# Kernel optimization log

Hardware: AMD Instinct MI355X
Metric: run time of the kernel (lower is better)

Reference implementation:

```python
import jax, jax.numpy as jnp
import numpy as np

EPS = 1e-5

def conv2d(x, w, b=None, stride=1, pad=0):
    # x: NCHW, w: OIHW
    y = jax.lax.conv_general_dilated(x, w, (stride, stride), [(pad, pad), (pad, pad)],
                                     dimension_numbers=('NCHW', 'OIHW', 'NCHW'))
    if b is not None:
        y = y + b[None, :, None, None]
    return y

def bn_eval(x, g, b, m, v):
    inv = jax.lax.rsqrt(v + EPS)
    return (x - m[None, :, None, None]) * (g * inv)[None, :, None, None] + b[None, :, None, None]

def setup_inputs() -> dict:
    key = jax.random.key(0)
    ks = jax.random.split(key, 20)
    B, Cin, Cout, H, W = 2, 64, 64, 96, 96
    Cqk = Cout // 4
    d = {}
    d['x'] = jax.random.normal(ks[0], (B, Cin, H, W), jnp.float32)
    # pre_conv: 3x3 conv (no bias) + BN + ReLU
    d['w_pre'] = jax.random.normal(ks[1], (Cout, Cin, 3, 3), jnp.float32) * 0.05
    d['bn1_g'] = jax.random.normal(ks[2], (Cout,), jnp.float32) * 0.1 + 1.0
    d['bn1_b'] = jax.random.normal(ks[3], (Cout,), jnp.float32) * 0.1
    d['bn1_m'] = jax.random.normal(ks[4], (Cout,), jnp.float32) * 0.1
    d['bn1_v'] = jax.random.uniform(ks[5], (Cout,), jnp.float32) + 0.5
    # 1x1 q/k/v convs (with bias, as nn.Conv2d default)
    d['wq'] = jax.random.normal(ks[6], (Cqk, Cout, 1, 1), jnp.float32) * 0.05
    d['bq'] = jax.random.normal(ks[7], (Cqk,), jnp.float32) * 0.01
    d['wk'] = jax.random.normal(ks[8], (Cqk, Cout, 1, 1), jnp.float32) * 0.05
    d['bk'] = jax.random.normal(ks[9], (Cqk,), jnp.float32) * 0.01
    d['wv'] = jax.random.normal(ks[10], (Cout, Cout, 1, 1), jnp.float32) * 0.05
    d['bv'] = jax.random.normal(ks[11], (Cout,), jnp.float32) * 0.01
    # final_conv: 3x3 conv (no bias) + BN + ReLU
    d['w_fin'] = jax.random.normal(ks[12], (Cout, Cout, 3, 3), jnp.float32) * 0.05
    d['bn2_g'] = jax.random.normal(ks[13], (Cout,), jnp.float32) * 0.1 + 1.0
    d['bn2_b'] = jax.random.normal(ks[14], (Cout,), jnp.float32) * 0.1
    d['bn2_m'] = jax.random.normal(ks[15], (Cout,), jnp.float32) * 0.1
    d['bn2_v'] = jax.random.uniform(ks[16], (Cout,), jnp.float32) + 0.5
    d['gamma'] = jnp.array([0.5], jnp.float32)  # nonzero so attention path contributes
    return d

def reference(x, w_pre, bn1_g, bn1_b, bn1_m, bn1_v, wq, bq, wk, bk, wv, bv,
              w_fin, bn2_g, bn2_b, bn2_m, bn2_v, gamma):
    # pre_conv: Conv3x3 + BN(eval) + ReLU
    x = jax.nn.relu(bn_eval(conv2d(x, w_pre, None, 1, 1), bn1_g, bn1_b, bn1_m, bn1_v))
    B, C, H, W = x.shape
    N = H * W
    q = conv2d(x, wq, bq).reshape(B, -1, N)   # (B, C/4, N)
    k = conv2d(x, wk, bk).reshape(B, -1, N)   # (B, C/4, N)
    v = conv2d(x, wv, bv).reshape(B, C, N)    # (B, C, N)
    energy = jnp.einsum('bci,bcj->bij', q, k)         # (B, N, N)
    attn = jax.nn.softmax(energy, axis=-1)
    # out[b,c,i] = sum_j v[b,c,j] * attn[b,i,j]  (bmm(V, attn^T) in torch)
    out = jnp.einsum('bcj,bij->bci', v, attn).reshape(B, C, H, W)
    out_feat = gamma[0] * out + x
    out_feat = jax.nn.relu(bn_eval(conv2d(out_feat, w_fin, None, 1, 1), bn2_g, bn2_b, bn2_m, bn2_v))
    return out_feat
```

## Files before the change

### kernel.cpp

```cpp
#include <hip/hip_runtime.h>
#include <hip/hip_bf16.h>


using short8 = __attribute__((ext_vector_type(8))) short;
using f32x4  = __attribute__((ext_vector_type(4))) float;
using f32x16 = __attribute__((ext_vector_type(16))) float;
using u32x4  = __attribute__((ext_vector_type(4))) unsigned;
typedef unsigned u32;
typedef unsigned short ushort;

#define NPIX 9216
#define PW 98
#define PLANE 9604
#define PLANEB 9608
#define SEG 240
#define LOG2E 1.44269504088896340736f

__device__ __forceinline__ ushort f2bf(float f) {
  u32 x = __builtin_bit_cast(u32, f);
  return (ushort)((x + 0x7fffu + ((x >> 16) & 1u)) >> 16);
}
__device__ __forceinline__ float bf2f(ushort h) {
  return __builtin_bit_cast(float, (u32)h << 16);
}

__global__ __launch_bounds__(256) void wprep(
    const float* __restrict__ w_pre, const float* __restrict__ w_fin,
    ushort* __restrict__ fpre, ushort* __restrict__ ffin)
{
  const int i = blockIdx.x * 256 + threadIdx.x;
  const float* w = blockIdx.y ? w_fin : w_pre;
  ushort* dst    = blockIdx.y ? ffin : fpre;
  const int kk = i & 7, l = (i >> 3) & 63, cot = (i >> 9) & 1;
  const int chunk = (i >> 10) & 3, tap = i >> 12;
  const int co = cot * 32 + (l & 31);
  const int ci = chunk * 16 + 8 * (l >> 5) + kk;
  const float wv = w[co * 576 + ci * 9 + tap];
  const ushort h = f2bf(wv);
  const ushort lo = f2bf(wv - bf2f(h));
  const int base = tap * 8192 + chunk * 2048 + cot * 1024 + l * 8 + kk;
  dst[base] = h;
  dst[base + 512] = lo;
}

__global__ __launch_bounds__(256) void pad_split(
    const float* __restrict__ in, ushort* __restrict__ xh, ushort* __restrict__ xl)
{
  const int plane = blockIdx.x;
  const float* src = in + (size_t)plane * 9216;
  const size_t dbase = (size_t)plane * PLANEB;
  for (int idx = threadIdx.x; idx < 9216; idx += 256) {
    const int y = idx / 96, x = idx - y * 96;
    const float v = src[idx];
    const ushort h = f2bf(v);
    const size_t d = dbase + (y + 1) * PW + x + 1;
    xh[d] = h;
    xl[d] = f2bf(v - bf2f(h));
  }
}

template <bool PADOUT>
__global__ __launch_bounds__(128) void conv3x3_mfma(
    const ushort* __restrict__ xh, const ushort* __restrict__ xl,
    const ushort* __restrict__ wfrag,
    const float* __restrict__ gg, const float* __restrict__ bb_,
    const float* __restrict__ mm, const float* __restrict__ vv,
    float* __restrict__ outp)
{
  __shared__ ushort stage[2][SEG][18];
  __shared__ float scb[64], shb[64];
  const int n0  = blockIdx.x * 32;
  const int b   = blockIdx.y;
  const int tid = threadIdx.x;
  const int wm  = tid >> 6;
  const int lane = tid & 63;
  const int li = lane & 31, hi = lane >> 5;

  if (tid < 64) {
    const float sc = gg[tid] * rsqrtf(vv[tid] + 1e-5f);
    scb[tid] = sc;
    shb[tid] = bb_[tid] - mm[tid] * sc;
  }

  f32x16 acc = {};
  const int sbase = n0 - 8;

  for (int chunk = 0; chunk < 4; ++chunk) {
    __syncthreads();
#pragma unroll
    for (int it = 0; it < 8; ++it) {
      const int item = tid + it * 128;
      if (item < 960) {
        const int pl   = item >= 480;
        const int rem  = pl ? item - 480 : item;
        const int eblk = rem >> 4;
        const int ci   = rem & 15;
        const ushort* src = (pl ? xl : xh) +
            (size_t)(b * 64 + chunk * 16 + ci) * PLANEB + sbase + eblk * 8;
        const short8 v = *(const short8*)src;
#pragma unroll
        for (int j = 0; j < 8; ++j) stage[pl][eblk * 8 + j][ci] = (ushort)v[j];
      }
    }
    __syncthreads();

    const ushort* wb0 = wfrag + (size_t)(chunk * 2048 + wm * 1024 + lane * 8);
    short8 ah = *(const short8*)(wb0);
    short8 al = *(const short8*)(wb0 + 512);
#pragma unroll
    for (int tap = 0; tap < 9; ++tap) {
      const int eoff = (tap / 3) * PW + (tap % 3) + 7 + li;
      const short8 bh = *(const short8*)&stage[0][eoff][hi * 8];
      const short8 bl = *(const short8*)&stage[1][eoff][hi * 8];
      short8 ahn, aln;
      if (tap < 8) {
        const ushort* wbn = wb0 + (size_t)(tap + 1) * 8192;
        ahn = *(const short8*)(wbn);
        aln = *(const short8*)(wbn + 512);
      }
      acc = __builtin_amdgcn_mfma_f32_32x32x16_bf16(ah, bh, acc, 0, 0, 0);
      acc = __builtin_amdgcn_mfma_f32_32x32x16_bf16(ah, bl, acc, 0, 0, 0);
      acc = __builtin_amdgcn_mfma_f32_32x32x16_bf16(al, bh, acc, 0, 0, 0);
      acc = __builtin_amdgcn_mfma_f32_32x32x16_bf16(al, bl, acc, 0, 0, 0);
      if (tap < 8) { ah = ahn; al = aln; }
    }
  }

  const int pix = n0 + li;
  const int y = pix / PW;
  const int x = pix - y * PW;
  if (x >= 1 && x <= 96) {
#pragma unroll
    for (int r = 0; r < 16; ++r) {
      const int co = wm * 32 + (r & 3) + 8 * (r >> 2) + 4 * hi;
      const float val = fmaxf(scb[co] * acc[r] + shb[co], 0.f);
      if (PADOUT)
        outp[(size_t)(b * 64 + co) * PLANE + pix + PW] = val;
      else
        outp[(size_t)(b * 64 + co) * 9216 + y * 96 + (x - 1)] = val;
    }
  }
}

__global__ __launch_bounds__(64) void qkv_kernel(
    const float* __restrict__ x1p,
    const float* __restrict__ wq, const float* __restrict__ bq,
    const float* __restrict__ wk, const float* __restrict__ bk,
    const float* __restrict__ wv, const float* __restrict__ bv,
    ushort* __restrict__ qsp, ushort* __restrict__ ksp,
    ushort* __restrict__ vfrag)
{
  const int pix0 = blockIdx.x * 16;
  const int cot  = blockIdx.y;
  const int b    = blockIdx.z;
  const int lane = threadIdx.x;
  const int g    = lane >> 4;
  const int col  = lane & 15;

  const float* wr;
  const float* bias;
  if (cot == 0)      { wr = wq + col * 64; bias = bq; }
  else if (cot == 1) { wr = wk + col * 64; bias = bk; }
  else               { wr = wv + ((cot - 2) * 16 + col) * 64; bias = bv + (cot - 2) * 16; }

  const int yy = pix0 / 96, xx = pix0 - yy * 96;
  const int ro = (yy + 1) * PW + xx + 1;

  f32x4 acc = (f32x4){0.f, 0.f, 0.f, 0.f};
  const float* xb = x1p + (size_t)b * 64 * PLANE;
#pragma unroll
  for (int kt = 0; kt < 2; ++kt) {
    const float4 wa = *(const float4*)(wr + kt * 32 + 8 * g);
    const float4 wb2 = *(const float4*)(wr + kt * 32 + 8 * g + 4);
    short8 af;
    af[0] = (short)f2bf(wa.x); af[1] = (short)f2bf(wa.y);
    af[2] = (short)f2bf(wa.z); af[3] = (short)f2bf(wa.w);
    af[4] = (short)f2bf(wb2.x); af[5] = (short)f2bf(wb2.y);
    af[6] = (short)f2bf(wb2.z); af[7] = (short)f2bf(wb2.w);
    short8 bf;
#pragma unroll
    for (int jj = 0; jj < 8; ++jj)
      bf[jj] = (short)f2bf(xb[(size_t)(kt * 32 + 8 * g + jj) * PLANE + ro + col]);
    acc = __builtin_amdgcn_mfma_f32_16x16x32_bf16(af, bf, acc, 0, 0, 0);
  }
  if (cot < 2) {
    ushort* dst = (cot == 0 ? qsp : ksp) + ((size_t)(b * NPIX + pix0 + col)) * 32;
    const float scl = (cot == 0) ? LOG2E : 1.f;
#pragma unroll
    for (int r = 0; r < 4; ++r) {
      const int cl = 4 * g + r;
      const float val = (acc[r] + bias[cl]) * scl;
      const ushort h = f2bf(val);
      dst[cl] = h;
      dst[16 + cl] = f2bf(val - bf2f(h));
    }
  } else {
    ushort* dst = vfrag + (size_t)b * 589824;
    const int pix = pix0 + col;
    const int jt = pix >> 5, ks = (pix >> 4) & 1;
    const int lhalf = 32 * ((pix >> 3) & 1);
    const int kk = pix & 7;
#pragma unroll
    for (int r = 0; r < 4; ++r) {
      const int cl = 4 * g + r;
      const int c = (cot - 2) * 16 + cl;
      const int h = c >> 5;
      const int lA = (c & 31) + lhalf;
      dst[(size_t)((((jt * 2 + h) * 2 + ks) * 64 + lA)) * 8 + kk] =
          f2bf(acc[r] + bias[cl]);
    }
  }
}

__global__ __launch_bounds__(256, 3) void attn_kernel(
    const ushort* __restrict__ qsp, const ushort* __restrict__ ksp,
    const ushort* __restrict__ vfrag, const float* __restrict__ x1p,
    const float* __restrict__ gamma_p,
    ushort* __restrict__ ofh, ushort* __restrict__ ofl)
{
  __shared__ float2 mlb[4][32];
  __shared__ float obuf[32][65];
  __shared__ float lbuf[32];

  const int b   = blockIdx.y;
  const int i0  = blockIdx.x * 32;
  const int tid = threadIdx.x;
  const int w   = tid >> 6;
  const int lane = tid & 63;
  const int li  = lane & 31;
  const int hi  = lane >> 5;

  for (int idx = tid; idx < 32 * 65; idx += 256) ((float*)obuf)[idx] = 0.f;
  if (tid < 32) lbuf[tid] = 0.f;
  __syncthreads();

  const ushort* kb    = ksp + (size_t)b * NPIX * 32;
  const ushort* vbase = vfrag + (size_t)b * 589824;

  const ushort* qrow = qsp + ((size_t)b * NPIX + i0 + li) * 32 + 8 * hi;
  const short8 qfh = *(const short8*)(qrow);
  const short8 qfl = *(const short8*)(qrow + 16);

  float m = -INFINITY;
  float lsum = 0.f;
  f32x16 acc[2] = {};

  const int jt0 = w * 72;
  const ushort* kptr = kb + (size_t)(jt0 * 32 + li) * 32 + 8 * hi;
  const ushort* vptr = vbase + ((size_t)(jt0 * 4) * 64 + lane) * 8;

  short8 kfh  = *(const short8*)kptr;
  short8 kfl  = *(const short8*)(kptr + 16);
  short8 vf00 = *(const short8*)(vptr);
  short8 vf01 = *(const short8*)(vptr + 512);
  short8 vf10 = *(const short8*)(vptr + 1024);
  short8 vf11 = *(const short8*)(vptr + 1536);

  const f32x16 zf = {};
  for (int t = 0; t < 72; ++t) {
    f32x16 s = __builtin_amdgcn_mfma_f32_32x32x16_bf16(kfh, qfh, zf, 0, 0, 0);
    s = __builtin_amdgcn_mfma_f32_32x32x16_bf16(kfl, qfh, s, 0, 0, 0);
    s = __builtin_amdgcn_mfma_f32_32x32x16_bf16(kfh, qfl, s, 0, 0, 0);

    short8 kfh_n, kfl_n, v00n, v01n, v10n, v11n;
    if (t < 71) {
      kptr += 1024; vptr += 2048;
      kfh_n = *(const short8*)kptr;
      kfl_n = *(const short8*)(kptr + 16);
      v00n = *(const short8*)(vptr);
      v01n = *(const short8*)(vptr + 512);
      v10n = *(const short8*)(vptr + 1024);
      v11n = *(const short8*)(vptr + 1536);
    }

    float pm = fmaxf(fmaxf(fmaxf(s[0], s[1]), fmaxf(s[2], s[3])),
                     fmaxf(fmaxf(s[4], s[5]), fmaxf(s[6], s[7])));
    pm = fmaxf(pm, fmaxf(fmaxf(fmaxf(s[8], s[9]), fmaxf(s[10], s[11])),
                         fmaxf(fmaxf(s[12], s[13]), fmaxf(s[14], s[15]))));
    {
      float o = pm;
      asm("v_permlane32_swap_b32 %0, %1" : "+v"(o), "+v"(pm));
      pm = fmaxf(pm, o);
    }

    if (__any(pm > m + 8.f)) {
      const float mnew = fmaxf(m, pm);
      const float corr = __builtin_amdgcn_exp2f(m - mnew);
      lsum *= corr;
      acc[0] *= corr;
      acc[1] *= corr;
      m = mnew;
    }

#pragma unroll
    for (int r = 0; r < 16; ++r) s[r] = __builtin_amdgcn_exp2f(s[r] - m);
    float ps = (((s[0] + s[1]) + (s[2] + s[3])) + ((s[4] + s[5]) + (s[6] + s[7]))) +
               (((s[8] + s[9]) + (s[10] + s[11])) + ((s[12] + s[13]) + (s[14] + s[15])));
    {
      float o = ps;
      asm("v_permlane32_swap_b32 %0, %1" : "+v"(o), "+v"(ps));
      ps = ps + o;
    }
    lsum += ps;

    u32 c01, c23, c45, c67, d01, d23, d45, d67;
    asm("v_cvt_pk_bf16_f32 %0, %1, %2" : "=v"(c01) : "v"(s[0]),  "v"(s[1]));
    asm("v_cvt_pk_bf16_f32 %0, %1, %2" : "=v"(c23) : "v"(s[2]),  "v"(s[3]));
    asm("v_cvt_pk_bf16_f32 %0, %1, %2" : "=v"(c45) : "v"(s[4]),  "v"(s[5]));
    asm("v_cvt_pk_bf16_f32 %0, %1, %2" : "=v"(c67) : "v"(s[6]),  "v"(s[7]));
    asm("v_cvt_pk_bf16_f32 %0, %1, %2" : "=v"(d01) : "v"(s[8]),  "v"(s[9]));
    asm("v_cvt_pk_bf16_f32 %0, %1, %2" : "=v"(d23) : "v"(s[10]), "v"(s[11]));
    asm("v_cvt_pk_bf16_f32 %0, %1, %2" : "=v"(d45) : "v"(s[12]), "v"(s[13]));
    asm("v_cvt_pk_bf16_f32 %0, %1, %2" : "=v"(d67) : "v"(s[14]), "v"(s[15]));
    asm("v_permlane32_swap_b32 %0, %1" : "+v"(c45), "+v"(c01));
    asm("v_permlane32_swap_b32 %0, %1" : "+v"(c67), "+v"(c23));
    asm("v_permlane32_swap_b32 %0, %1" : "+v"(d45), "+v"(d01));
    asm("v_permlane32_swap_b32 %0, %1" : "+v"(d67), "+v"(d23));
    const short8 pf1 = __builtin_bit_cast(short8, (u32x4){c01, c23, c45, c67});
    const short8 pf2 = __builtin_bit_cast(short8, (u32x4){d01, d23, d45, d67});

    acc[0] = __builtin_amdgcn_mfma_f32_32x32x16_bf16(vf00, pf1, acc[0], 0, 0, 0);
    acc[0] = __builtin_amdgcn_mfma_f32_32x32x16_bf16(vf01, pf2, acc[0], 0, 0, 0);
    acc[1] = __builtin_amdgcn_mfma_f32_32x32x16_bf16(vf10, pf1, acc[1], 0, 0, 0);
    acc[1] = __builtin_amdgcn_mfma_f32_32x32x16_bf16(vf11, pf2, acc[1], 0, 0, 0);

    if (t < 71) {
      kfh = kfh_n; kfl = kfl_n;
      vf00 = v00n; vf01 = v01n; vf10 = v10n; vf11 = v11n;
    }
  }

  if (hi == 0) { float2 t2; t2.x = m; t2.y = lsum; mlb[w][li] = t2; }
  __syncthreads();
  float M = -INFINITY;
#pragma unroll
  for (int ww = 0; ww < 4; ++ww) M = fmaxf(M, mlb[ww][li].x);
  const float f = __builtin_amdgcn_exp2f(m - M);
  if (hi == 0) atomicAdd(&lbuf[li], lsum * f);
#pragma unroll
  for (int hh = 0; hh < 2; ++hh)
#pragma unroll
    for (int r = 0; r < 16; ++r) {
      const int c = (r & 3) + 8 * (r >> 2) + 4 * hi + 32 * hh;
      atomicAdd(&obuf[li][c], acc[hh][r] * f);
    }
  __syncthreads();

  const float gm = gamma_p[0];
  for (int idx = tid; idx < 2048; idx += 256) {
    const int il = idx & 31, c = idx >> 5;
    const int p = i0 + il;
    const int y = p / 96, x = p - y * 96;
    const int ro = (y + 1) * PW + x + 1;
    const float val = obuf[il][c] / lbuf[il] * gm +
                      x1p[(size_t)(b * 64 + c) * PLANE + ro];
    const ushort h = f2bf(val);
    const size_t d = (size_t)(b * 64 + c) * PLANEB + ro;
    ofh[d] = h;
    ofl[d] = f2bf(val - bf2f(h));
  }
}

extern "C" void kernel_launch(void* const* d_in, const int* in_sizes, int n_in,
                              void* d_out, int out_size, void* d_ws, size_t ws_size,
                              hipStream_t stream) {
  const float* x      = (const float*)d_in[0];
  const float* w_pre  = (const float*)d_in[1];
  const float* bn1_g  = (const float*)d_in[2];
  const float* bn1_b  = (const float*)d_in[3];
  const float* bn1_m  = (const float*)d_in[4];
  const float* bn1_v  = (const float*)d_in[5];
  const float* wq     = (const float*)d_in[6];
  const float* bq     = (const float*)d_in[7];
  const float* wk     = (const float*)d_in[8];
  const float* bk     = (const float*)d_in[9];
  const float* wv     = (const float*)d_in[10];
  const float* bv     = (const float*)d_in[11];
  const float* w_fin  = (const float*)d_in[12];
  const float* bn2_g  = (const float*)d_in[13];
  const float* bn2_b  = (const float*)d_in[14];
  const float* bn2_m  = (const float*)d_in[15];
  const float* bn2_v  = (const float*)d_in[16];
  const float* gamma  = (const float*)d_in[17];
  float* out = (float*)d_out;

  char* ws = (char*)d_ws;
  float*  x1p  = (float*)(ws);
  ushort* xh   = (ushort*)(ws + 4917248);
  ushort* xl   = (ushort*)(ws + 7376896);
  ushort* qsp  = (ushort*)(ws + 9836544);
  ushort* ksp  = (ushort*)(ws + 11016192);
  ushort* vfr  = (ushort*)(ws + 12195840);
  ushort* fpre = (ushort*)(ws + 14555136);
  ushort* ffin = (ushort*)(ws + 14702592);
  ushort* ofh = xh;
  ushort* ofl = xl;

  hipMemsetAsync(ws + 4917248, 0, 4919296, stream);

  wprep<<<dim3(144, 2), 256, 0, stream>>>(w_pre, w_fin, fpre, ffin);
  pad_split<<<dim3(128), 256, 0, stream>>>(x, xh, xl);
  conv3x3_mfma<true><<<dim3(294, 2), 128, 0, stream>>>(
      xh, xl, fpre, bn1_g, bn1_b, bn1_m, bn1_v, x1p);
  qkv_kernel<<<dim3(576, 6, 2), 64, 0, stream>>>(
      x1p, wq, bq, wk, bk, wv, bv, qsp, ksp, vfr);
  attn_kernel<<<dim3(288, 2), 256, 0, stream>>>(
      qsp, ksp, vfr, x1p, gamma, ofh, ofl);
  conv3x3_mfma<false><<<dim3(294, 2), 128, 0, stream>>>(
      ofh, ofl, ffin, bn2_g, bn2_b, bn2_m, bn2_v, out);
}
```

Measured before the change: 164.7 us.

## Software-pipeline QK MFMA one tile ahead and use max3 for row max

Restructures the attention loop so the QK^T MFMAs for the next key tile are issued before the softmax of the current tile, letting matrix-core work overlap the exp/max/convert VALU work. K fragments are now prefetched two tiles ahead to feed this. The row-max reduction also switches to v_max3_f32 to cut VALU instruction count. This raises register pressure (an extra f32x16 accumulator and extra K fragments), which could reduce occupancy or cause spills.

```diff
diff --git a/kernel.cpp b/kernel.cpp
--- a/kernel.cpp
+++ b/kernel.cpp
@@ -22,6 +22,11 @@
 }
 __device__ __forceinline__ float bf2f(ushort h) {
   return __builtin_bit_cast(float, (u32)h << 16);
+}
+__device__ __forceinline__ float max3f(float a, float b, float c) {
+  float d;
+  asm("v_max3_f32 %0, %1, %2, %3" : "=v"(d) : "v"(a), "v"(b), "v"(c));
+  return d;
 }
 
 __global__ __launch_bounds__(256) void wprep(
@@ -249,34 +254,52 @@
   const ushort* kptr = kb + (size_t)(jt0 * 32 + li) * 32 + 8 * hi;
   const ushort* vptr = vbase + ((size_t)(jt0 * 4) * 64 + lane) * 8;
 
-  short8 kfh  = *(const short8*)kptr;
-  short8 kfl  = *(const short8*)(kptr + 16);
+  const f32x16 zf = {};
+
+  short8 kh0 = *(const short8*)kptr;
+  short8 kl0 = *(const short8*)(kptr + 16);
+  f32x16 s = __builtin_amdgcn_mfma_f32_32x32x16_bf16(kh0, qfh, zf, 0, 0, 0);
+  s = __builtin_amdgcn_mfma_f32_32x32x16_bf16(kl0, qfh, s, 0, 0, 0);
+  s = __builtin_amdgcn_mfma_f32_32x32x16_bf16(kh0, qfl, s, 0, 0, 0);
+  kptr += 1024;
+  short8 kh_n = *(const short8*)kptr;
+  short8 kl_n = *(const short8*)(kptr + 16);
   short8 vf00 = *(const short8*)(vptr);
   short8 vf01 = *(const short8*)(vptr + 512);
   short8 vf10 = *(const short8*)(vptr + 1024);
   short8 vf11 = *(const short8*)(vptr + 1536);
 
-  const f32x16 zf = {};
   for (int t = 0; t < 72; ++t) {
-    f32x16 s = __builtin_amdgcn_mfma_f32_32x32x16_bf16(kfh, qfh, zf, 0, 0, 0);
-    s = __builtin_amdgcn_mfma_f32_32x32x16_bf16(kfl, qfh, s, 0, 0, 0);
-    s = __builtin_amdgcn_mfma_f32_32x32x16_bf16(kfh, qfl, s, 0, 0, 0);
-
-    short8 kfh_n, kfl_n, v00n, v01n, v10n, v11n;
+    f32x16 s_next;
     if (t < 71) {
-      kptr += 1024; vptr += 2048;
-      kfh_n = *(const short8*)kptr;
-      kfl_n = *(const short8*)(kptr + 16);
+      s_next = __builtin_amdgcn_mfma_f32_32x32x16_bf16(kh_n, qfh, zf, 0, 0, 0);
+      s_next = __builtin_amdgcn_mfma_f32_32x32x16_bf16(kl_n, qfh, s_next, 0, 0, 0);
+      s_next = __builtin_amdgcn_mfma_f32_32x32x16_bf16(kh_n, qfl, s_next, 0, 0, 0);
+    }
+
+    short8 kh_p, kl_p, v00n, v01n, v10n, v11n;
+    if (t < 70) {
+      kptr += 1024;
+      kh_p = *(const short8*)kptr;
+      kl_p = *(const short8*)(kptr + 16);
+    }
+    if (t < 71) {
+      vptr += 2048;
       v00n = *(const short8*)(vptr);
       v01n = *(const short8*)(vptr + 512);
       v10n = *(const short8*)(vptr + 1024);
       v11n = *(const short8*)(vptr + 1536);
     }
 
-    float pm = fmaxf(fmaxf(fmaxf(s[0], s[1]), fmaxf(s[2], s[3])),
-                     fmaxf(fmaxf(s[4], s[5]), fmaxf(s[6], s[7])));
-    pm = fmaxf(pm, fmaxf(fmaxf(fmaxf(s[8], s[9]), fmaxf(s[10], s[11])),
-                         fmaxf(fmaxf(s[12], s[13]), fmaxf(s[14], s[15]))));
+    float pm, q1, q2, q3, q4;
+    pm = max3f(s[0], s[1], s[2]);
+    q1 = max3f(s[3], s[4], s[5]);
+    q2 = max3f(s[6], s[7], s[8]);
+    q3 = max3f(s[9], s[10], s[11]);
+    q4 = max3f(s[12], s[13], s[14]);
+    pm = max3f(pm, q1, q2);
+    pm = max3f(pm, q3, q4);
+    pm = fmaxf(pm, s[15]);
     {
       float o = pm;
       asm("v_permlane32_swap_b32 %0, %1" : "+v"(o), "+v"(pm));
@@ -325,9 +348,10 @@
     acc[1] = __builtin_amdgcn_mfma_f32_32x32x16_bf16(vf11, pf2, acc[1], 0, 0, 0);
 
     if (t < 71) {
-      kfh = kfh_n; kfl = kfl_n;
+      s = s_next;
       vf00 = v00n; vf01 = v01n; vf10 = v10n; vf11 = v11n;
     }
+    if (t < 70) { kh_n = kh_p; kl_n = kl_p; }
   }
 
   if (hi == 0) { float2 t2; t2.x = m; t2.y = lsum; mlb[w][li] = t2; }
```

After: 163.7 us. No clear change (-0.6%).

## Process two key tiles per attention iteration with max3 reductions

Applied to the files above, without the earlier changes.

Unrolls the attention loop by two, so each iteration computes scores for two 32-key tiles and shares one online-softmax max/rescale step between them. The row max now uses v_max3_f32. V fragments are loaded at the top of each iteration rather than prefetched from the previous one, and occupancy is lowered from 3 to 2 blocks per CU. The aim is to cut per-tile softmax overhead and give the scheduler more independent MFMA work, at the cost of more registers, fewer resident waves and less explicit latency hiding for the V loads.

```diff
diff --git a/kernel.cpp b/kernel.cpp
--- a/kernel.cpp
+++ b/kernel.cpp
@@ -22,6 +22,11 @@
 }
 __device__ __forceinline__ float bf2f(ushort h) {
   return __builtin_bit_cast(float, (u32)h << 16);
+}
+__device__ __forceinline__ float max3f(float a, float b, float c) {
+  float d;
+  asm("v_max3_f32 %0, %1, %2, %3" : "=v"(d) : "v"(a), "v"(b), "v"(c));
+  return d;
 }
 
 __global__ __launch_bounds__(256) void wprep(
@@ -212,7 +217,7 @@
   }
 }
 
-__global__ __launch_bounds__(256, 3) void attn_kernel(
+__global__ __launch_bounds__(256, 2) void attn_kernel(
     const ushort* __restrict__ qsp, const ushort* __restrict__ ksp,
     const ushort* __restrict__ vfrag, const float* __restrict__ x1p,
     const float* __restrict__ gamma_p,
@@ -249,34 +254,55 @@
   const ushort* kptr = kb + (size_t)(jt0 * 32 + li) * 32 + 8 * hi;
   const ushort* vptr = vbase + ((size_t)(jt0 * 4) * 64 + lane) * 8;
 
-  short8 kfh  = *(const short8*)kptr;
-  short8 kfl  = *(const short8*)(kptr + 16);
-  short8 vf00 = *(const short8*)(vptr);
-  short8 vf01 = *(const short8*)(vptr + 512);
-  short8 vf10 = *(const short8*)(vptr + 1024);
-  short8 vf11 = *(const short8*)(vptr + 1536);
-
   const f32x16 zf = {};
-  for (int t = 0; t < 72; ++t) {
-    f32x16 s = __builtin_amdgcn_mfma_f32_32x32x16_bf16(kfh, qfh, zf, 0, 0, 0);
-    s = __builtin_amdgcn_mfma_f32_32x32x16_bf16(kfl, qfh, s, 0, 0, 0);
-    s = __builtin_amdgcn_mfma_f32_32x32x16_bf16(kfh, qfl, s, 0, 0, 0);
-
-    short8 kfh_n, kfl_n, v00n, v01n, v10n, v11n;
-    if (t < 71) {
-      kptr += 1024; vptr += 2048;
-      kfh_n = *(const short8*)kptr;
-      kfl_n = *(const short8*)(kptr + 16);
-      v00n = *(const short8*)(vptr);
-      v01n = *(const short8*)(vptr + 512);
-      v10n = *(const short8*)(vptr + 1024);
-      v11n = *(const short8*)(vptr + 1536);
-    }
-
-    float pm = fmaxf(fmaxf(fmaxf(s[0], s[1]), fmaxf(s[2], s[3])),
-                     fmaxf(fmaxf(s[4], s[5]), fmaxf(s[6], s[7])));
-    pm = fmaxf(pm, fmaxf(fmaxf(fmaxf(s[8], s[9]), fmaxf(s[10], s[11])),
-                         fmaxf(fmaxf(s[12], s[13]), fmaxf(s[14], s[15]))));
+
+  short8 kh0 = *(const short8*)kptr;
+  short8 kl0 = *(const short8*)(kptr + 16);
+  short8 kh1 = *(const short8*)(kptr + 1024);
+  short8 kl1 = *(const short8*)(kptr + 1040);
+
+  for (int t = 0; t < 36; ++t) {
+    short8 vA0 = *(const short8*)(vptr);
+    short8 vA1 = *(const short8*)(vptr + 512);
+    short8 vA2 = *(const short8*)(vptr + 1024);
+    short8 vA3 = *(const short8*)(vptr + 1536);
+    short8 vB0 = *(const short8*)(vptr + 2048);
+    short8 vB1 = *(const short8*)(vptr + 2560);
+    short8 vB2 = *(const short8*)(vptr + 3072);
+    short8 vB3 = *(const short8*)(vptr + 3584);
+
+    f32x16 s0 = __builtin_amdgcn_mfma_f32_32x32x16_bf16(kh0, qfh, zf, 0, 0, 0);
+    s0 = __builtin_amdgcn_mfma_f32_32x32x16_bf16(kl0, qfh, s0, 0, 0, 0);
+    s0 = __builtin_amdgcn_mfma_f32_32x32x16_bf16(kh0, qfl, s0, 0, 0, 0);
+    f32x16 s1 = __builtin_amdgcn_mfma_f32_32x32x16_bf16(kh1, qfh, zf, 0, 0, 0);
+    s1 = __builtin_amdgcn_mfma_f32_32x32x16_bf16(kl1, qfh, s1, 0, 0, 0);
+    s1 = __builtin_amdgcn_mfma_f32_32x32x16_bf16(kh1, qfl, s1, 0, 0, 0);
+
+    if (t < 35) {
+      kptr += 2048;
+      kh0 = *(const short8*)kptr;
+      kl0 = *(const short8*)(kptr + 16);
+      kh1 = *(const short8*)(kptr + 1024);
+      kl1 = *(const short8*)(kptr + 1040);
+    }
+    if (t < 35) vptr += 4096;
+
+    float p0 = max3f(s0[0], s0[1], s0[2]);
+    float p1 = max3f(s0[3], s0[4], s0[5]);
+    float p2 = max3f(s0[6], s0[7], s0[8]);
+    float p3 = max3f(s0[9], s0[10], s0[11]);
+    float p4 = max3f(s0[12], s0[13], s0[14]);
+    float p5 = max3f(s1[0], s1[1], s1[2]);
+    float p6 = max3f(s1[3], s1[4], s1[5]);
+    float p7 = max3f(s1[6], s1[7], s1[8]);
+    float p8 = max3f(s1[9], s1[10], s1[11]);
+    float p9 = max3f(s1[12], s1[13], s1[14]);
+    float pa = fmaxf(s0[15], s1[15]);
+    p0 = max3f(p0, p1, p2);
+    p3 = max3f(p3, p4, p5);
+    p6 = max3f(p6, p7, p8);
+    p9 = max3f(p9, pa, p0);
+    float pm = max3f(p3, p6, p9);
     {
       float o = pm;
       asm("v_permlane32_swap_b32 %0, %1" : "+v"(o), "+v"(pm));
@@ -293,9 +319,13 @@
     }
 
 #pragma unroll
-    for (int r = 0; r < 16; ++r) s[r] = __builtin_amdgcn_exp2f(s[r] - m);
-    float ps = (((s[0] + s[1]) + (s[2] + s[3])) + ((s[4] + s[5]) + (s[6] + s[7]))) +
-               (((s[8] + s[9]) + (s[10] + s[11])) + ((s[12] + s[13]) + (s[14] + s[15])));
+    for (int r = 0; r < 16; ++r) s0[r] = __builtin_amdgcn_exp2f(s0[r] - m);
+#pragma unroll
+    for (int r = 0; r < 16; ++r) s1[r] = __builtin_amdgcn_exp2f(s1[r] - m);
+    float ps = ((((s0[0] + s0[1]) + (s0[2] + s0[3])) + ((s0[4] + s0[5]) + (s0[6] + s0[7]))) +
+                (((s0[8] + s0[9]) + (s0[10] + s0[11])) + ((s0[12] + s0[13]) + (s0[14] + s0[15])))) +
+               ((((s1[0] + s1[1]) + (s1[2] + s1[3])) + ((s1[4] + s1[5]) + (s1[6] + s1[7]))) +
+                (((s1[8] + s1[9]) + (s1[10] + s1[11])) + ((s1[12] + s1[13]) + (s1[14] + s1[15]))));
     {
       float o = ps;
       asm("v_permlane32_swap_b32 %0, %1" : "+v"(o), "+v"(ps));
@@ -303,31 +333,45 @@
     }
     lsum += ps;
 
+    u32 a01, a23, a45, a67, b01, b23, b45, b67;
     u32 c01, c23, c45, c67, d01, d23, d45, d67;
-    asm("v_cvt_pk_bf16_f32 %0, %1, %2" : "=v"(c01) : "v"(s[0]),  "v"(s[1]));
-    asm("v_cvt_pk_bf16_f32 %0, %1, %2" : "=v"(c23) : "v"(s[2]),  "v"(s[3]));
-    asm("v_cvt_pk_bf16_f32 %0, %1, %2" : "=v"(c45) : "v"(s[4]),  "v"(s[5]));
-    asm("v_cvt_pk_bf16_f32 %0, %1, %2" : "=v"(c67) : "v"(s[6]),  "v"(s[7]));
-    asm("v_cvt_pk_bf16_f32 %0, %1, %2" : "=v"(d01) : "v"(s[8]),  "v"(s[9]));
-    asm("v_cvt_pk_bf16_f32 %0, %1, %2" : "=v"(d23) : "v"(s[10]), "v"(s[11]));
-    asm("v_cvt_pk_bf16_f32 %0, %1, %2" : "=v"(d45) : "v"(s[12]), "v"(s[13]));
-    asm("v_cvt_pk_bf16_f32 %0, %1, %2" : "=v"(d67) : "v"(s[14]), "v"(s[15]));
+    asm("v_cvt_pk_bf16_f32 %0, %1, %2" : "=v"(a01) : "v"(s0[0]),  "v"(s0[1]));
+    asm("v_cvt_pk_bf16_f32 %0, %1, %2" : "=v"(a23) : "v"(s0[2]),  "v"(s0[3]));
+    asm("v_cvt_pk_bf16_f32 %0, %1, %2" : "=v"(a45) : "v"(s0[4]),  "v"(s0[5]));
+    asm("v_cvt_pk_bf16_f32 %0, %1, %2" : "=v"(a67) : "v"(s0[6]),  "v"(s0[7]));
+    asm("v_cvt_pk_bf16_f32 %0, %1, %2" : "=v"(b01) : "v"(s0[8]),  "v"(s0[9]));
+    asm("v_cvt_pk_bf16_f32 %0, %1, %2" : "=v"(b23) : "v"(s0[10]), "v"(s0[11]));
+    asm("v_cvt_pk_bf16_f32 %0, %1, %2" : "=v"(b45) : "v"(s0[12]), "v"(s0[13]));
+    asm("v_cvt_pk_bf16_f32 %0, %1, %2" : "=v"(b67) : "v"(s0[14]), "v"(s0[15]));
+    asm("v_permlane32_swap_b32 %0, %1" : "+v"(a45), "+v"(a01));
+    asm("v_permlane32_swap_b32 %0, %1" : "+v"(a67), "+v"(a23));
+    asm("v_permlane32_swap_b32 %0, %1" : "+v"(b45), "+v"(b01));
+    asm("v_permlane32_swap_b32 %0, %1" : "+v"(b67), "+v"(b23));
+    asm("v_cvt_pk_bf16_f32 %0, %1, %2" : "=v"(c01) : "v"(s1[0]),  "v"(s1[1]));
+    asm("v_cvt_pk_bf16_f32 %0, %1, %2" : "=v"(c23) : "v"(s1[2]),  "v"(s1[3]));
+    asm("v_cvt_pk_bf16_f32 %0, %1, %2" : "=v"(c45) : "v"(s1[4]),  "v"(s1[5]));
+    asm("v_cvt_pk_bf16_f32 %0, %1, %2" : "=v"(c67) : "v"(s1[6]),  "v"(s1[7]));
+    asm("v_cvt_pk_bf16_f32 %0, %1, %2" : "=v"(d01) : "v"(s1[8]),  "v"(s1[9]));
+    asm("v_cvt_pk_bf16_f32 %0, %1, %2" : "=v"(d23) : "v"(s1[10]), "v"(s1[11]));
+    asm("v_cvt_pk_bf16_f32 %0, %1, %2" : "=v"(d45) : "v"(s1[12]), "v"(s1[13]));
+    asm("v_cvt_pk_bf16_f32 %0, %1, %2" : "=v"(d67) : "v"(s1[14]), "v"(s1[15]));
     asm("v_permlane32_swap_b32 %0, %1" : "+v"(c45), "+v"(c01));
     asm("v_permlane32_swap_b32 %0, %1" : "+v"(c67), "+v"(c23));
     asm("v_permlane32_swap_b32 %0, %1" : "+v"(d45), "+v"(d01));
     asm("v_permlane32_swap_b32 %0, %1" : "+v"(d67), "+v"(d23));
-    const short8 pf1 = __builtin_bit_cast(short8, (u32x4){c01, c23, c45, c67});
-    const short8 pf2 = __builtin_bit_cast(short8, (u32x4){d01, d23, d45, d67});
-
-    acc[0] = __builtin_amdgcn_mfma_f32_32x32x16_bf16(vf00, pf1, acc[0], 0, 0, 0);
-    acc[0] = __builtin_amdgcn_mfma_f32_32x32x16_bf16(vf01, pf2, acc[0], 0, 0, 0);
-    acc[1] = __builtin_amdgcn_mfma_f32_32x32x16_bf16(vf10, pf1, acc[1], 0, 0, 0);
-    acc[1] = __builtin_amdgcn_mfma_f32_32x32x16_bf16(vf11, pf2, acc[1], 0, 0, 0);
-
-    if (t < 71) {
-      kfh = kfh_n; kfl = kfl_n;
-      vf00 = v00n; vf01 = v01n; vf10 = v10n; vf11 = v11n;
-    }
+    const short8 pfA1 = __builtin_bit_cast(short8, (u32x4){a01, a23, a45, a67});
+    const short8 pfA2 = __builtin_bit_cast(short8, (u32x4){b01, b23, b45, b67});
+    const short8 pfB1 = __builtin_bit_cast(short8, (u32x4){c01, c23, c45, c67});
+    const short8 pfB2 = __builtin_bit_cast(short8, (u32x4){d01, d23, d45, d67});
+
+    acc[0] = __builtin_amdgcn_mfma_f32_32x32x16_bf16(vA0, pfA1, acc[0], 0, 0, 0);
+    acc[0] = __builtin_amdgcn_mfma_f32_32x32x16_bf16(vA1, pfA2, acc[0], 0, 0, 0);
+    acc[1] = __builtin_amdgcn_mfma_f32_32x32x16_bf16(vA2, pfA1, acc[1], 0, 0, 0);
+    acc[1] = __builtin_amdgcn_mfma_f32_32x32x16_bf16(vA3, pfA2, acc[1], 0, 0, 0);
+    acc[0] = __builtin_amdgcn_mfma_f32_32x32x16_bf16(vB0, pfB1, acc[0], 0, 0, 0);
+    acc[0] = __builtin_amdgcn_mfma_f32_32x32x16_bf16(vB1, pfB2, acc[0], 0, 0, 0);
+    acc[1] = __builtin_amdgcn_mfma_f32_32x32x16_bf16(vB2, pfB1, acc[1], 0, 0, 0);
+    acc[1] = __builtin_amdgcn_mfma_f32_32x32x16_bf16(vB3, pfB2, acc[1], 0, 0, 0);
   }
 
   if (hi == 0) { float2 t2; t2.x = m; t2.y = lsum; mlb[w][li] = t2; }
```

Result: slower. 168.6 us (+2.4%).
